# Kernel tuning notes

Measured on AMD Instinct MI355X. Metric: run time of the kernel, lower is better.

The kernel has to match this reference:

```python
import jax, jax.numpy as jnp
import numpy as np

B, NQ, C = 2, 16384, 768
NH, NL, NP = 6, 1, 4
HW = 128
D = C // NH  # 128, deform_ratio = 1.0
EPS = 1e-6


def layernorm(x, g, b):
    m = jnp.mean(x, -1, keepdims=True)
    v = jnp.var(x, -1, keepdims=True)
    return (x - m) * jax.lax.rsqrt(v + EPS) * g + b


def setup_inputs() -> dict:
    key = jax.random.key(0)
    ks = jax.random.split(key, 16)
    n = lambda k, s, sc=1.0: jax.random.normal(k, s, jnp.float32) * sc
    return {
        "query": n(ks[0], (B, NQ, C)),
        "reference_points": jax.random.uniform(ks[1], (B, NQ, NL, 2), jnp.float32),
        "feat": n(ks[2], (B, NQ, C)),
        "spatial_shapes": jnp.array([[HW, HW]], jnp.int32),
        "level_start_index": jnp.array([0], jnp.int32),
        "qn_g": jnp.ones((C,), jnp.float32), "qn_b": jnp.zeros((C,), jnp.float32),
        "fn_g": jnp.ones((C,), jnp.float32), "fn_b": jnp.zeros((C,), jnp.float32),
        "gamma": n(ks[3], (C,), 0.1),
        "W_off": n(ks[4], (C, NH * NL * NP * 2), 0.02), "b_off": n(ks[5], (NH * NL * NP * 2,), 0.5),
        "W_attn": n(ks[6], (C, NH * NL * NP), 0.02), "b_attn": jnp.zeros((NH * NL * NP,), jnp.float32),
        "W_val": n(ks[7], (C, NH * D), 0.02), "b_val": jnp.zeros((NH * D,), jnp.float32),
        "W_out": n(ks[8], (NH * D, C), 0.02), "b_out": jnp.zeros((C,), jnp.float32),
    }


def _ms_deform_attn(q, rp, f, W_off, b_off, W_attn, b_attn, W_val, b_val, W_out, b_out, shapes, starts):
    Bq, Nq, _ = q.shape
    value = (f @ W_val + b_val).reshape(Bq, -1, NH, D)  # (B, Lin, H, D)
    off = (q @ W_off + b_off).reshape(Bq, Nq, NH, NL, NP, 2)
    aw = jax.nn.softmax((q @ W_attn + b_attn).reshape(Bq, Nq, NH, NL * NP), -1)
    aw = aw.reshape(Bq, Nq, NH, NL, NP)
    shapes_f = jnp.asarray(shapes, q.dtype)
    normalizer = jnp.stack([shapes_f[:, 1], shapes_f[:, 0]], -1)  # (NL, 2) = (W, H)
    loc = rp[:, :, None, :, None, :] + off / normalizer[None, None, None, :, None, :]
    out = jnp.zeros((Bq, Nq, NH, D), q.dtype)
    b_idx = jnp.arange(Bq)[:, None, None, None]
    h_idx = jnp.arange(NH)[None, None, :, None]
    for l in range(NL):
        Hl, Wl = int(shapes[l, 0]), int(shapes[l, 1])
        s = int(starts[l])
        v = value[:, s:s + Hl * Wl].reshape(Bq, Hl, Wl, NH, D)
        ll = loc[:, :, :, l]                        # (B, Nq, H, P, 2)
        # grid_sample bilinear, align_corners=False, zero padding
        x = ll[..., 0] * Wl - 0.5
        y = ll[..., 1] * Hl - 0.5
        x0 = jnp.floor(x); y0 = jnp.floor(y)
        x1 = x0 + 1.0;     y1 = y0 + 1.0
        wx1 = x - x0; wx0 = 1.0 - wx1
        wy1 = y - y0; wy0 = 1.0 - wy1
        def corner(xi, yi, w):
            valid = (xi >= 0) & (xi <= Wl - 1) & (yi >= 0) & (yi <= Hl - 1)
            xc = jnp.clip(xi, 0, Wl - 1).astype(jnp.int32)
            yc = jnp.clip(yi, 0, Hl - 1).astype(jnp.int32)
            g = v[b_idx, yc, xc, h_idx]             # (B, Nq, H, P, D)
            return g * (w * valid)[..., None]
        samp = (corner(x0, y0, wx0 * wy0) + corner(x1, y0, wx1 * wy0)
                + corner(x0, y1, wx0 * wy1) + corner(x1, y1, wx1 * wy1))
        out = out + jnp.einsum('bqhpd,bqhp->bqhd', samp, aw[:, :, :, l])
    return out.reshape(Bq, Nq, NH * D) @ W_out + b_out


def reference(query, reference_points, feat, spatial_shapes, level_start_index,
              qn_g, qn_b, fn_g, fn_b, gamma,
              W_off, b_off, W_attn, b_attn, W_val, b_val, W_out, b_out):
    shapes = np.asarray(spatial_shapes)
    starts = np.asarray(level_start_index)
    q = layernorm(query, qn_g, qn_b)
    f = layernorm(feat, fn_g, fn_b)
    attn = _ms_deform_attn(q, reference_points, f, W_off, b_off, W_attn, b_attn,
                           W_val, b_val, W_out, b_out, shapes, starts)
    return query + gamma * attn
```

## Files before the change

kernel.cpp:

```cpp
#include <hip/hip_runtime.h>
#include <stdint.h>

typedef unsigned short u16;
typedef float f32x4 __attribute__((ext_vector_type(4)));
typedef short s16x8 __attribute__((ext_vector_type(8)));

#define K_DIM 768
#define M_ROWS 32768
#define NQ_ 16384
#define HW_ 128

__device__ __forceinline__ float bf2f(u16 u) {
    union { uint32_t u; float f; } c; c.u = ((uint32_t)u) << 16; return c.f;
}
__device__ __forceinline__ u16 f2bf(float f) {
    union { float f; uint32_t u; } c; c.f = f;
    uint32_t u = c.u;
    u += 0x7FFFu + ((u >> 16) & 1);
    return (u16)(u >> 16);
}

__device__ __forceinline__ void gload_lds16(const void* g, void* l) {
    __builtin_amdgcn_global_load_lds((const __attribute__((address_space(1))) void*)g,
                                     (__attribute__((address_space(3))) void*)l, 16, 0, 0);
}

__global__ void prep_all_kernel(const float* __restrict__ Wval, const float* __restrict__ Wout,
                                const float* __restrict__ Woff, const float* __restrict__ Wattn,
                                const float* __restrict__ boff, const float* __restrict__ battn,
                                u16* __restrict__ wv_t, u16* __restrict__ wo_t,
                                u16* __restrict__ woa_t, float* __restrict__ bias) {
    int idx = blockIdx.x * 256 + threadIdx.x;
    const int SZ = 768 * K_DIM;
    if (idx < SZ) {
        int n = idx / K_DIM, k = idx - n * K_DIM;
        wv_t[idx] = f2bf(Wval[(size_t)k * 768 + n]);
    } else if (idx < 2 * SZ) {
        int r = idx - SZ;
        int n = r / K_DIM, k = r - n * K_DIM;
        wo_t[r] = f2bf(Wout[(size_t)k * 768 + n]);
    } else if (idx < 2 * SZ + 128 * K_DIM) {
        int r = idx - 2 * SZ;
        int n = r / K_DIM, k = r - n * K_DIM;
        float v = 0.0f;
        if (n < 48)      v = Woff[(size_t)k * 48 + n];
        else if (n < 72) v = Wattn[(size_t)k * 24 + (n - 48)];
        woa_t[r] = f2bf(v);
        if (r < 128) bias[r] = r < 48 ? boff[r] : (r < 72 ? battn[r - 48] : 0.0f);
    }
}

__global__ __launch_bounds__(192) void ln_kernel(const float* __restrict__ x,
                                                 const float* __restrict__ g,
                                                 const float* __restrict__ b,
                                                 u16* __restrict__ out) {
    int row = blockIdx.x;
    int tid = threadIdx.x;
    const float4 v = ((const float4*)(x + (size_t)row * K_DIM))[tid];
    float s  = v.x + v.y + v.z + v.w;
    float s2 = v.x * v.x + v.y * v.y + v.z * v.z + v.w * v.w;
#pragma unroll
    for (int off = 32; off >= 1; off >>= 1) {
        s  += __shfl_down(s, off);
        s2 += __shfl_down(s2, off);
    }
    __shared__ float red[6];
    int wv = tid >> 6, lane = tid & 63;
    if (lane == 0) { red[wv] = s; red[3 + wv] = s2; }
    __syncthreads();
    s  = red[0] + red[1] + red[2];
    s2 = red[3] + red[4] + red[5];
    float mean = s * (1.0f / K_DIM);
    float var  = s2 * (1.0f / K_DIM) - mean * mean;
    float inv  = rsqrtf(var + 1e-6f);
    const float4 gg = ((const float4*)g)[tid];
    const float4 bb = ((const float4*)b)[tid];
    ushort4 o;
    o.x = f2bf((v.x - mean) * inv * gg.x + bb.x);
    o.y = f2bf((v.y - mean) * inv * gg.y + bb.y);
    o.z = f2bf((v.z - mean) * inv * gg.z + bb.z);
    o.w = f2bf((v.w - mean) * inv * gg.w + bb.w);
    ((ushort4*)(out + (size_t)row * K_DIM))[tid] = o;
}

#define EP_VAL 0
#define EP_OA 1
#define EP_FINAL 2

template <int EP, int NX, int BN = 128>
__global__ __launch_bounds__(512) void gemm_kernel(
        const u16* __restrict__ A, const u16* __restrict__ Bt,
        const float* __restrict__ bias, void* __restrict__ out, int ld_out,
        const float* __restrict__ query, const float* __restrict__ gamma) {
    constexpr int NF = BN / 64;
    constexpr int BCH = BN / 64;
    constexpr int BUF = 16384 + BN * 128;
    constexpr int NWG = NX * (M_ROWS / 128);
    constexpr int CPX = NWG / 8;
    __shared__ __align__(16) char smem[2 * BUF];
    const int lane = threadIdx.x & 63;
    const int wv = threadIdx.x >> 6;
    const int wr = wv >> 2, wc = wv & 3;
    const int lr = lane & 15, lg = lane >> 4;
    const int wg  = blockIdx.x;
    const int swz = (wg & 7) * CPX + (wg >> 3);
    const int m0 = (swz / NX) * 128;
    const int n0 = (swz % NX) * BN;

    f32x4 acc[4][NF] = {};

    const u16* Ab = A + (size_t)m0 * K_DIM;
    const u16* Bb = Bt + (size_t)n0 * K_DIM;

    auto stage = [&](char* buf, int kt) {
#pragma unroll
        for (int c = 0; c < 2; ++c) {
            int chunk = wv * 2 + c;
            int row = chunk * 8 + (lane >> 3);
            int slot = (lane & 7) ^ (row & 7);
            gload_lds16(Ab + (size_t)row * K_DIM + kt + slot * 8, buf + chunk * 1024);
        }
#pragma unroll
        for (int c = 0; c < BCH; ++c) {
            int chunk = wv * BCH + c;
            int row = chunk * 8 + (lane >> 3);
            int slot = (lane & 7) ^ (row & 7);
            gload_lds16(Bb + (size_t)row * K_DIM + kt + slot * 8, buf + 16384 + chunk * 1024);
        }
    };

    stage(smem, 0);
    asm volatile("s_waitcnt vmcnt(0)" ::: "memory");
    __builtin_amdgcn_s_barrier();
    __builtin_amdgcn_sched_barrier(0);

    constexpr int NT = K_DIM / 64;
    int cur = 0;
#pragma unroll 2
    for (int t = 0; t < NT; ++t) {
        const char* rb = smem + cur * BUF;
        if (t + 1 < NT) stage(smem + (cur ^ 1) * BUF, (t + 1) * 64);
#pragma unroll
        for (int kk = 0; kk < 2; ++kk) {
            s16x8 af[4], bfr[NF];
#pragma unroll
            for (int m = 0; m < 4; ++m) {
                int row = wr * 64 + m * 16 + lr;
                int slot = (kk * 4 + lg) ^ (row & 7);
                af[m] = *(const s16x8*)(rb + row * 128 + slot * 16);
            }
#pragma unroll
            for (int n = 0; n < NF; ++n) {
                int row = wc * (BN / 4) + n * 16 + lr;
                int slot = (kk * 4 + lg) ^ (row & 7);
                bfr[n] = *(const s16x8*)(rb + 16384 + row * 128 + slot * 16);
            }
            __builtin_amdgcn_s_setprio(1);
#pragma unroll
            for (int m = 0; m < 4; ++m)
#pragma unroll
                for (int n = 0; n < NF; ++n)
                    acc[m][n] = __builtin_amdgcn_mfma_f32_16x16x32_bf16(af[m], bfr[n], acc[m][n], 0, 0, 0);
            __builtin_amdgcn_s_setprio(0);
        }
        asm volatile("s_waitcnt vmcnt(0)" ::: "memory");
        __builtin_amdgcn_s_barrier();
        __builtin_amdgcn_sched_barrier(0);
        cur ^= 1;
    }

#pragma unroll
    for (int m = 0; m < 4; ++m) {
#pragma unroll
        for (int r = 0; r < 4; ++r) {
            int row = m0 + wr * 64 + m * 16 + lg * 4 + r;
#pragma unroll
            for (int n = 0; n < NF; ++n) {
                int col = n0 + wc * (BN / 4) + n * 16 + lr;
                float v = acc[m][n][r] + bias[col];
                if constexpr (EP == EP_VAL) {
                    ((u16*)out)[((size_t)(col >> 7) * M_ROWS + row) * 128 + (col & 127)] = f2bf(v);
                } else if constexpr (EP == EP_OA) {
                    if (col < 72) {
                        int hh, s;
                        if (col < 48) { hh = col >> 3; s = col & 7; }
                        else          { hh = (col - 48) >> 2; s = 8 + ((col - 48) & 3); }
                        ((float*)out)[((size_t)hh * M_ROWS + row) * 12 + s] = v;
                    }
                } else {
                    size_t idx = (size_t)row * ld_out + col;
                    ((float*)out)[idx] = query[idx] + gamma[col] * v;
                }
            }
        }
    }
}

__global__ __launch_bounds__(512) void sample_kernel(
        const float* __restrict__ oa2,
        const float* __restrict__ rp,
        const u16* __restrict__ value,
        u16* __restrict__ samp) {
    const int h = blockIdx.x >> 12;
    const int q = __builtin_amdgcn_readfirstlane(
                      ((blockIdx.x & 4095) << 3) + (threadIdx.x >> 6));
    const int lane = threadIdx.x & 63;
    const int b = q >> 14;
    const float* oar = oa2 + ((size_t)h * M_ROWS + q) * 12;

    const int p  = (lane >> 2) & 3;
    const int cn = lane & 3;
    const float lp = oar[8 + p];
    const float e  = __expf(lp);
    float es = e;
    es += __shfl_xor(es, 4);
    es += __shfl_xor(es, 8);
    const float aw = e * __builtin_amdgcn_rcpf(es);

    const float2 offv = *(const float2*)(oar + p * 2);
    const float2 rpv  = *(const float2*)(rp + (size_t)q * 2);
    const float xx = rpv.x * 128.0f + offv.x - 0.5f;
    const float yy = rpv.y * 128.0f + offv.y - 0.5f;
    const float x0 = floorf(xx), y0 = floorf(yy);
    const float fx = xx - x0, fy = yy - y0;
    const float cx = x0 + (float)(cn & 1);
    const float cy = y0 + (float)(cn >> 1);
    const float wx = (cn & 1) ? fx : 1.0f - fx;
    const float wy = (cn >> 1) ? fy : 1.0f - fy;
    const bool valid = (cx >= 0.0f) & (cx <= 127.0f) & (cy >= 0.0f) & (cy <= 127.0f);
    const float w = valid ? aw * wx * wy : 0.0f;
    const int cxi = (int)fminf(fmaxf(cx, 0.0f), 127.0f);
    const int cyi = (int)fminf(fmaxf(cy, 0.0f), 127.0f);
    const int packed = (__float_as_int(w) & 0xffff0000) | (cyi * HW_ + cxi);

    const char* vbs = (const char*)value + ((size_t)h * M_ROWS + (size_t)b * NQ_) * 256;
    float acc0 = 0.0f, acc1 = 0.0f;
#pragma unroll
    for (int c = 0; c < 16; ++c) {
        const int pc = __builtin_amdgcn_readlane(packed, c);
        const float wc = __int_as_float(pc & 0xffff0000);
        const int   oc = (pc & 0x3fff) << 8;
        const uint32_t d = ((const uint32_t*)(vbs + oc))[lane];
        acc0 = fmaf(wc, __int_as_float(d << 16), acc0);
        acc1 = fmaf(wc, __int_as_float(d), acc1);
    }
    ushort2 o; o.x = f2bf(acc0); o.y = f2bf(acc1);
    ((ushort2*)(samp + (size_t)q * K_DIM + h * 128))[lane] = o;
}

extern "C" void kernel_launch(void* const* d_in, const int* in_sizes, int n_in,
                              void* d_out, int out_size, void* d_ws, size_t ws_size,
                              hipStream_t stream) {
    (void)in_sizes; (void)n_in; (void)out_size; (void)ws_size;
    const float* query  = (const float*)d_in[0];
    const float* rp     = (const float*)d_in[1];
    const float* feat   = (const float*)d_in[2];
    const float* qn_g   = (const float*)d_in[5];
    const float* qn_b   = (const float*)d_in[6];
    const float* fn_g   = (const float*)d_in[7];
    const float* fn_b   = (const float*)d_in[8];
    const float* gamma  = (const float*)d_in[9];
    const float* W_off  = (const float*)d_in[10];
    const float* b_off  = (const float*)d_in[11];
    const float* W_attn = (const float*)d_in[12];
    const float* b_attn = (const float*)d_in[13];
    const float* W_val  = (const float*)d_in[14];
    const float* b_val  = (const float*)d_in[15];
    const float* W_out  = (const float*)d_in[16];
    const float* b_out  = (const float*)d_in[17];

    char* ws = (char*)d_ws;
    u16*   ln_buf  = (u16*)  (ws + 0);
    u16*   val_buf = (u16*)  (ws + 50331648);
    float* oa2_buf = (float*)(ws + 100663296);
    u16*   wv_t    = (u16*)  (ws + 117440512);
    u16*   wo_t    = (u16*)  (ws + 118620160);
    u16*   woa_t   = (u16*)  (ws + 119799808);
    float* bias_oa = (float*)(ws + 119996416);
    u16*   samp_buf = ln_buf;

    prep_all_kernel<<<(2 * 768 * 768 + 128 * 768 + 255) / 256, 256, 0, stream>>>(
        W_val, W_out, W_off, W_attn, b_off, b_attn, wv_t, wo_t, woa_t, bias_oa);

    ln_kernel<<<M_ROWS, 192, 0, stream>>>(feat, fn_g, fn_b, ln_buf);

    gemm_kernel<EP_VAL, 6><<<6 * (M_ROWS / 128), 512, 0, stream>>>(ln_buf, wv_t, b_val, val_buf, 768, nullptr, nullptr);

    ln_kernel<<<M_ROWS, 192, 0, stream>>>(query, qn_g, qn_b, ln_buf);

    gemm_kernel<EP_OA, 2, 64><<<2 * (M_ROWS / 128), 512, 0, stream>>>(ln_buf, woa_t, bias_oa, oa2_buf, 0, nullptr, nullptr);

    sample_kernel<<<6 * 4096, 512, 0, stream>>>(oa2_buf, rp, val_buf, samp_buf);

    gemm_kernel<EP_FINAL, 6><<<6 * (M_ROWS / 128), 512, 0, stream>>>(samp_buf, wo_t, b_out, d_out, 768, query, gamma);
}
```

Measured before the change: 246.8 us.

## Use 32x32x16 MFMA tiles in GEMMs and wave-per-row layernorm

The GEMM kernel moves from 16x16x32 bf16 MFMA fragments to 32x32x16 ones, with each wave owning a 32-column strip and 64 or 32 rows depending on BN. The epilogue is rewritten to match the new accumulator layout. The layernorm kernel now processes one row per wave, four rows per block, with xor shuffles and no shared-memory reduction or block barrier. Larger MFMA tiles cut LDS fragment reads per flop, but the epilogue's store pattern changes and more registers are used.

Result: faster. 240.1 us (-2.7%).

```diff
diff --git a/kernel.cpp b/kernel.cpp
--- a/kernel.cpp
+++ b/kernel.cpp
@@ -2,7 +2,7 @@
 #include <stdint.h>
 
 typedef unsigned short u16;
-typedef float f32x4 __attribute__((ext_vector_type(4)));
+typedef float f32x16 __attribute__((ext_vector_type(16)));
 typedef short s16x8 __attribute__((ext_vector_type(8)));
 
 #define K_DIM 768
@@ -50,37 +50,39 @@
     }
 }
 
-__global__ __launch_bounds__(192) void ln_kernel(const float* __restrict__ x,
+__global__ __launch_bounds__(256) void ln_kernel(const float* __restrict__ x,
                                                  const float* __restrict__ g,
                                                  const float* __restrict__ b,
                                                  u16* __restrict__ out) {
-    int row = blockIdx.x;
-    int tid = threadIdx.x;
-    const float4 v = ((const float4*)(x + (size_t)row * K_DIM))[tid];
-    float s  = v.x + v.y + v.z + v.w;
-    float s2 = v.x * v.x + v.y * v.y + v.z * v.z + v.w * v.w;
+    const int row = blockIdx.x * 4 + (threadIdx.x >> 6);
+    const int lane = threadIdx.x & 63;
+    float4 v[3];
+    float s = 0.0f, s2 = 0.0f;
+#pragma unroll
+    for (int j = 0; j < 3; ++j) {
+        v[j] = ((const float4*)(x + (size_t)row * K_DIM))[lane + 64 * j];
+        s  += v[j].x + v[j].y + v[j].z + v[j].w;
+        s2 += v[j].x * v[j].x + v[j].y * v[j].y + v[j].z * v[j].z + v[j].w * v[j].w;
+    }
 #pragma unroll
     for (int off = 32; off >= 1; off >>= 1) {
-        s  += __shfl_down(s, off);
-        s2 += __shfl_down(s2, off);
-    }
-    __shared__ float red[6];
-    int wv = tid >> 6, lane = tid & 63;
-    if (lane == 0) { red[wv] = s; red[3 + wv] = s2; }
-    __syncthreads();
-    s  = red[0] + red[1] + red[2];
-    s2 = red[3] + red[4] + red[5];
-    float mean = s * (1.0f / K_DIM);
-    float var  = s2 * (1.0f / K_DIM) - mean * mean;
-    float inv  = rsqrtf(var + 1e-6f);
-    const float4 gg = ((const float4*)g)[tid];
-    const float4 bb = ((const float4*)b)[tid];
-    ushort4 o;
-    o.x = f2bf((v.x - mean) * inv * gg.x + bb.x);
-    o.y = f2bf((v.y - mean) * inv * gg.y + bb.y);
-    o.z = f2bf((v.z - mean) * inv * gg.z + bb.z);
-    o.w = f2bf((v.w - mean) * inv * gg.w + bb.w);
-    ((ushort4*)(out + (size_t)row * K_DIM))[tid] = o;
+        s  += __shfl_xor(s, off);
+        s2 += __shfl_xor(s2, off);
+    }
+    const float mean = s * (1.0f / K_DIM);
+    const float var  = s2 * (1.0f / K_DIM) - mean * mean;
+    const float inv  = rsqrtf(var + 1e-6f);
+#pragma unroll
+    for (int j = 0; j < 3; ++j) {
+        const float4 gg = ((const float4*)g)[lane + 64 * j];
+        const float4 bb = ((const float4*)b)[lane + 64 * j];
+        ushort4 o;
+        o.x = f2bf((v[j].x - mean) * inv * gg.x + bb.x);
+        o.y = f2bf((v[j].y - mean) * inv * gg.y + bb.y);
+        o.z = f2bf((v[j].z - mean) * inv * gg.z + bb.z);
+        o.w = f2bf((v[j].w - mean) * inv * gg.w + bb.w);
+        ((ushort4*)(out + (size_t)row * K_DIM))[lane + 64 * j] = o;
+    }
 }
 
 #define EP_VAL 0
@@ -92,7 +94,10 @@
         const u16* __restrict__ A, const u16* __restrict__ Bt,
         const float* __restrict__ bias, void* __restrict__ out, int ld_out,
         const float* __restrict__ query, const float* __restrict__ gamma) {
-    constexpr int NF = BN / 64;
+    constexpr int WN  = (BN >= 128) ? 4 : 2;
+    constexpr int WM  = 8 / WN;
+    constexpr int MW  = 128 / WM;
+    constexpr int MF  = MW / 32;
     constexpr int BCH = BN / 64;
     constexpr int BUF = 16384 + BN * 128;
     constexpr int NWG = NX * (M_ROWS / 128);
@@ -100,14 +105,14 @@
     __shared__ __align__(16) char smem[2 * BUF];
     const int lane = threadIdx.x & 63;
     const int wv = threadIdx.x >> 6;
-    const int wr = wv >> 2, wc = wv & 3;
-    const int lr = lane & 15, lg = lane >> 4;
+    const int wr = wv / WN, wc = wv % WN;
+    const int lr = lane & 31, hi = lane >> 5;
     const int wg  = blockIdx.x;
     const int swz = (wg & 7) * CPX + (wg >> 3);
     const int m0 = (swz / NX) * 128;
     const int n0 = (swz % NX) * BN;
 
-    f32x4 acc[4][NF] = {};
+    f32x16 acc[MF] = {};
 
     const u16* Ab = A + (size_t)m0 * K_DIM;
     const u16* Bb = Bt + (size_t)n0 * K_DIM;
@@ -141,26 +146,23 @@
         const char* rb = smem + cur * BUF;
         if (t + 1 < NT) stage(smem + (cur ^ 1) * BUF, (t + 1) * 64);
 #pragma unroll
-        for (int kk = 0; kk < 2; ++kk) {
-            s16x8 af[4], bfr[NF];
-#pragma unroll
-            for (int m = 0; m < 4; ++m) {
-                int row = wr * 64 + m * 16 + lr;
-                int slot = (kk * 4 + lg) ^ (row & 7);
-                af[m] = *(const s16x8*)(rb + row * 128 + slot * 16);
+        for (int kk = 0; kk < 4; ++kk) {
+            s16x8 af[MF], bfr;
+#pragma unroll
+            for (int mi = 0; mi < MF; ++mi) {
+                int row = wr * MW + mi * 32 + lr;
+                int slot = (kk * 2 + hi) ^ (row & 7);
+                af[mi] = *(const s16x8*)(rb + row * 128 + slot * 16);
             }
-#pragma unroll
-            for (int n = 0; n < NF; ++n) {
-                int row = wc * (BN / 4) + n * 16 + lr;
-                int slot = (kk * 4 + lg) ^ (row & 7);
-                bfr[n] = *(const s16x8*)(rb + 16384 + row * 128 + slot * 16);
+            {
+                int row = wc * 32 + lr;
+                int slot = (kk * 2 + hi) ^ (row & 7);
+                bfr = *(const s16x8*)(rb + 16384 + row * 128 + slot * 16);
             }
             __builtin_amdgcn_s_setprio(1);
 #pragma unroll
-            for (int m = 0; m < 4; ++m)
-#pragma unroll
-                for (int n = 0; n < NF; ++n)
-                    acc[m][n] = __builtin_amdgcn_mfma_f32_16x16x32_bf16(af[m], bfr[n], acc[m][n], 0, 0, 0);
+            for (int mi = 0; mi < MF; ++mi)
+                acc[mi] = __builtin_amdgcn_mfma_f32_32x32x16_bf16(af[mi], bfr, acc[mi], 0, 0, 0);
             __builtin_amdgcn_s_setprio(0);
         }
         asm volatile("s_waitcnt vmcnt(0)" ::: "memory");
@@ -169,28 +171,25 @@
         cur ^= 1;
     }
 
-#pragma unroll
-    for (int m = 0; m < 4; ++m) {
-#pragma unroll
-        for (int r = 0; r < 4; ++r) {
-            int row = m0 + wr * 64 + m * 16 + lg * 4 + r;
-#pragma unroll
-            for (int n = 0; n < NF; ++n) {
-                int col = n0 + wc * (BN / 4) + n * 16 + lr;
-                float v = acc[m][n][r] + bias[col];
-                if constexpr (EP == EP_VAL) {
-                    ((u16*)out)[((size_t)(col >> 7) * M_ROWS + row) * 128 + (col & 127)] = f2bf(v);
-                } else if constexpr (EP == EP_OA) {
-                    if (col < 72) {
-                        int hh, s;
-                        if (col < 48) { hh = col >> 3; s = col & 7; }
-                        else          { hh = (col - 48) >> 2; s = 8 + ((col - 48) & 3); }
-                        ((float*)out)[((size_t)hh * M_ROWS + row) * 12 + s] = v;
-                    }
-                } else {
-                    size_t idx = (size_t)row * ld_out + col;
-                    ((float*)out)[idx] = query[idx] + gamma[col] * v;
+    const int col = n0 + wc * 32 + lr;
+#pragma unroll
+    for (int mi = 0; mi < MF; ++mi) {
+#pragma unroll
+        for (int reg = 0; reg < 16; ++reg) {
+            int row = m0 + wr * MW + mi * 32 + (reg & 3) + 8 * (reg >> 2) + 4 * hi;
+            float v = acc[mi][reg] + bias[col];
+            if constexpr (EP == EP_VAL) {
+                ((u16*)out)[((size_t)(col >> 7) * M_ROWS + row) * 128 + (col & 127)] = f2bf(v);
+            } else if constexpr (EP == EP_OA) {
+                if (col < 72) {
+                    int hh, s;
+                    if (col < 48) { hh = col >> 3; s = col & 7; }
+                    else          { hh = (col - 48) >> 2; s = 8 + ((col - 48) & 3); }
+                    ((float*)out)[((size_t)hh * M_ROWS + row) * 12 + s] = v;
                 }
+            } else {
+                size_t idx = (size_t)row * ld_out + col;
+                ((float*)out)[idx] = query[idx] + gamma[col] * v;
             }
         }
     }
@@ -282,11 +281,11 @@
     prep_all_kernel<<<(2 * 768 * 768 + 128 * 768 + 255) / 256, 256, 0, stream>>>(
         W_val, W_out, W_off, W_attn, b_off, b_attn, wv_t, wo_t, woa_t, bias_oa);
 
-    ln_kernel<<<M_ROWS, 192, 0, stream>>>(feat, fn_g, fn_b, ln_buf);
+    ln_kernel<<<M_ROWS / 4, 256, 0, stream>>>(feat, fn_g, fn_b, ln_buf);
 
     gemm_kernel<EP_VAL, 6><<<6 * (M_ROWS / 128), 512, 0, stream>>>(ln_buf, wv_t, b_val, val_buf, 768, nullptr, nullptr);
 
-    ln_kernel<<<M_ROWS, 192, 0, stream>>>(query, qn_g, qn_b, ln_buf);
+    ln_kernel<<<M_ROWS / 4, 256, 0, stream>>>(query, qn_g, qn_b, ln_buf);
 
     gemm_kernel<EP_OA, 2, 64><<<2 * (M_ROWS / 128), 512, 0, stream>>>(ln_buf, woa_t, bias_oa, oa2_buf, 0, nullptr, nullptr);
 
```
